# Kernel optimization log

Hardware: AMD Instinct MI355X
Metric: run time of the kernel (lower is better)

Reference implementation:

```python
import jax, jax.numpy as jnp
import numpy as np

B, L, S, D, H = 2, 384, 384, 512, 256
BASE_TEMP = 10.0
LN_EPS = 1e-5


def setup_inputs() -> dict:
    key = jax.random.key(0)
    ks = jax.random.split(key, 12)
    return {
        "q": jax.random.normal(ks[0], (B, L, D), jnp.float32),
        "k": jax.random.normal(ks[1], (B, S, D), jnp.float32),
        "q_global": jax.random.normal(ks[2], (B, D), jnp.float32),
        "k_global": jax.random.normal(ks[3], (B, D), jnp.float32),
        "W1": jax.random.normal(ks[4], (4 * D, H), jnp.float32) * (1.0 / np.sqrt(4 * D)),
        "b1": jnp.zeros((H,), jnp.float32),
        "gamma": jnp.ones((H,), jnp.float32),
        "beta": jnp.zeros((H,), jnp.float32),
        "W2": jax.random.normal(ks[5], (H, 1), jnp.float32) * (1.0 / np.sqrt(H)),
        "b2": jnp.zeros((1,), jnp.float32),
        "gumbel_u": jax.random.uniform(ks[6], (B, L, S, 2), jnp.float32),
    }


def reference(q, k, q_global, k_global, W1, b1, gamma, beta, W2, b2, gumbel_u):
    d = q.shape[-1]
    # Decompose Linear(4D,H) on the [q, k, q_global, k_global] concat into
    # four per-tensor projections; sum broadcasts to the pairwise grid.
    Wq, Wk, Wqg, Wkg = jnp.split(W1, 4, axis=0)  # each [D,H]
    hq = q @ Wq + (q_global @ Wqg)[:, None, :]   # [B,L,H]
    hk = k @ Wk + (k_global @ Wkg)[:, None, :]   # [B,S,H]
    h = hq[:, :, None, :] + hk[:, None, :, :] + b1  # [B,L,S,H]
    h = jax.nn.gelu(h, approximate=False)
    mu = jnp.mean(h, axis=-1, keepdims=True)
    var = jnp.mean(jnp.square(h - mu), axis=-1, keepdims=True)
    h = (h - mu) * jax.lax.rsqrt(var + LN_EPS) * gamma + beta
    thresholds = (h @ W2)[..., 0] + b2[0]  # [B,L,S]
    sim = jnp.einsum("bld,bsd->bls", q, k) / jnp.sqrt(jnp.float32(d))
    logits = (sim - thresholds) / BASE_TEMP
    binary_logits = jnp.stack([-logits, logits], axis=-1)  # [B,L,S,2]
    u = jnp.clip(gumbel_u, 1e-6, 1.0 - 1e-6)
    g = -jnp.log(-jnp.log(u))
    soft = jax.nn.softmax(binary_logits + g, axis=-1)  # tau=1.0
    hard = jax.nn.one_hot(jnp.argmax(soft, axis=-1), 2, dtype=soft.dtype)
    y = hard + soft - jax.lax.stop_gradient(soft)  # straight-through
    return y[..., 1][:, None, :, :]  # [B,1,L,S]
```

## Files before the change

kernel.cpp:

```cpp
#include <hip/hip_runtime.h>
#include <hip/hip_bf16.h>
#include <math.h>

#define Bb 2
#define Lq 384
#define Sk 384
#define Dd 512
#define Hh 256

#define PROJ_ROWS 2
#define LIST_CAP 65536

#define HQD_OFF  0
#define HKD_OFF  (HQD_OFF + Bb*Lq*Hh*8)
#define GQD_OFF  (HKD_OFF + Bb*Sk*Hh*8)
#define GKD_OFF  (GQD_OFF + Bb*Hh*8)
#define HQ_OFF   (GKD_OFF + Bb*Hh*8)
#define HK_OFF   (HQ_OFF + Bb*Lq*Hh*4)
#define SIM0_OFF (HK_OFF + Bb*Sk*Hh*4)
#define SIM1_OFF (SIM0_OFF + Bb*Lq*Sk*4)
#define CNT_OFF  (SIM1_OFF + Bb*Lq*Sk*4)
#define LIST_OFF (CNT_OFF + 16)

__global__ __launch_bounds__(256) void globald_kernel(
    const float* __restrict__ qg, const float* __restrict__ kg,
    const float* __restrict__ W1,
    double* __restrict__ gq_d, double* __restrict__ gk_d)
{
    __shared__ double red[64][5];
    int bx  = blockIdx.x;
    int isK = bx & 1;
    int b   = (bx >> 1) & 1;
    int hc  = bx >> 2;
    int tid = threadIdx.x;
    int hl  = tid >> 2;
    int dp  = tid & 3;
    int h   = hc * 64 + hl;
    const float* gv = (isK ? kg : qg) + b * Dd;
    const float* wp = W1 + (isK ? 3 : 2) * Dd * Hh + h;
    int d0 = dp * 128;
    double a0 = 0, a1 = 0, a2 = 0, a3 = 0;
    for (int i = 0; i < 128; i += 4) {
        int d = d0 + i;
        a0 = fma((double)gv[d + 0], (double)wp[(d + 0) * Hh], a0);
        a1 = fma((double)gv[d + 1], (double)wp[(d + 1) * Hh], a1);
        a2 = fma((double)gv[d + 2], (double)wp[(d + 2) * Hh], a2);
        a3 = fma((double)gv[d + 3], (double)wp[(d + 3) * Hh], a3);
    }
    red[hl][dp] = ((a0 + a1) + (a2 + a3));
    __syncthreads();
    if (dp == 0) {
        double s = (red[hl][0] + red[hl][1]) + (red[hl][2] + red[hl][3]);
        (isK ? gk_d : gq_d)[b * Hh + h] = s;
    }
}

__global__ __launch_bounds__(256) void projd_kernel(
    const float* __restrict__ q, const float* __restrict__ k,
    const float* __restrict__ W1, const float* __restrict__ b1,
    const double* __restrict__ gq_d, const double* __restrict__ gk_d,
    double* __restrict__ hq_d, double* __restrict__ hk_d,
    float* __restrict__ hq, float* __restrict__ hk)
{
    __shared__ __align__(16) float tile[PROJ_ROWS][Dd];
    int tid = threadIdx.x;
    const int tpb  = Lq / PROJ_ROWS;
    const int half = Bb * tpb;
    int bx = blockIdx.x;
    bool isQ = bx < half;
    int bb = isQ ? bx : bx - half;
    int b  = bb / tpb;
    int rt = bb % tpb;
    const float*  src = isQ ? q : k;
    const double* gl  = isQ ? gq_d : gk_d;
    int woff = isQ ? 0 : Dd * Hh;
    double* dstd = isQ ? hq_d : hk_d;
    float*  dstf = isQ ? hq : hk;

    int base = (b * Lq + rt * PROJ_ROWS) * Dd;
    *reinterpret_cast<float4*>(&tile[0][0] + tid * 4) =
        *reinterpret_cast<const float4*>(src + base + tid * 4);
    double gd = gl[b * Hh + tid];
    __syncthreads();

    const float* wp = W1 + woff + tid;
    double acc0 = 0.0, acc1 = 0.0;
    for (int d4 = 0; d4 < Dd; d4 += 4) {
        double w0 = (double)wp[(d4 + 0) * Hh];
        double w1 = (double)wp[(d4 + 1) * Hh];
        double w2 = (double)wp[(d4 + 2) * Hh];
        double w3 = (double)wp[(d4 + 3) * Hh];
        float4 t0 = *reinterpret_cast<const float4*>(&tile[0][d4]);
        float4 t1 = *reinterpret_cast<const float4*>(&tile[1][d4]);
        acc0 = fma((double)t0.x, w0, acc0);
        acc0 = fma((double)t0.y, w1, acc0);
        acc0 = fma((double)t0.z, w2, acc0);
        acc0 = fma((double)t0.w, w3, acc0);
        acc1 = fma((double)t1.x, w0, acc1);
        acc1 = fma((double)t1.y, w1, acc1);
        acc1 = fma((double)t1.z, w2, acc1);
        acc1 = fma((double)t1.w, w3, acc1);
    }
    double b1d = isQ ? (double)b1[tid] : 0.0;
    int ob = (b * Lq + rt * PROJ_ROWS) * Hh + tid;
    double tot0 = acc0 + gd, tot1 = acc1 + gd;
    dstd[ob]      = tot0;
    dstd[ob + Hh] = tot1;
    dstf[ob]      = (float)(tot0 + b1d);
    dstf[ob + Hh] = (float)(tot1 + b1d);
}

__global__ __launch_bounds__(256) void sim_kernel(
    const float* __restrict__ q, const float* __restrict__ k,
    float* __restrict__ sim01)
{
    __shared__ __align__(16) float qs[32][132];
    __shared__ __align__(16) float ks[32][132];
    int tid = threadIdx.x;
    int bx = blockIdx.x;
    int kc = (bx >= Bb * 144) ? 1 : 0;
    int r  = bx - kc * Bb * 144;
    int b  = r / 144;  r %= 144;
    int lt = r / 12, st = r % 12;
    int tl = tid >> 4, ts = tid & 15;
    const float* qb = q + (b * Lq + lt * 32) * Dd;
    const float* kb = k + (b * Sk + st * 32) * Dd;
    float a00 = 0.f, a01 = 0.f, a10 = 0.f, a11 = 0.f;
    for (int c = kc * 256; c < kc * 256 + 256; c += 128) {
        __syncthreads();
        for (int i = tid; i < 1024; i += 256) {
            int row = i >> 5;
            int c4  = (i & 31) << 2;
            *reinterpret_cast<float4*>(&qs[row][c4]) =
                *reinterpret_cast<const float4*>(qb + row * Dd + c + c4);
            *reinterpret_cast<float4*>(&ks[row][c4]) =
                *reinterpret_cast<const float4*>(kb + row * Dd + c + c4);
        }
        __syncthreads();
#pragma unroll 2
        for (int dd = 0; dd < 128; dd += 4) {
            float4 q0 = *reinterpret_cast<const float4*>(&qs[tl][dd]);
            float4 q1 = *reinterpret_cast<const float4*>(&qs[tl + 16][dd]);
            float4 k0 = *reinterpret_cast<const float4*>(&ks[ts][dd]);
            float4 k1 = *reinterpret_cast<const float4*>(&ks[ts + 16][dd]);
            a00 = fmaf(q0.x, k0.x, a00); a00 = fmaf(q0.y, k0.y, a00);
            a00 = fmaf(q0.z, k0.z, a00); a00 = fmaf(q0.w, k0.w, a00);
            a01 = fmaf(q0.x, k1.x, a01); a01 = fmaf(q0.y, k1.y, a01);
            a01 = fmaf(q0.z, k1.z, a01); a01 = fmaf(q0.w, k1.w, a01);
            a10 = fmaf(q1.x, k0.x, a10); a10 = fmaf(q1.y, k0.y, a10);
            a10 = fmaf(q1.z, k0.z, a10); a10 = fmaf(q1.w, k0.w, a10);
            a11 = fmaf(q1.x, k1.x, a11); a11 = fmaf(q1.y, k1.y, a11);
            a11 = fmaf(q1.z, k1.z, a11); a11 = fmaf(q1.w, k1.w, a11);
        }
    }
    const float sc = 0.04419417382415922f;
    float* dst = sim01 + kc * (Bb * Lq * Sk);
    int l0 = lt * 32 + tl, s0 = st * 32 + ts;
    dst[(b * Lq + l0)      * Sk + s0]      = a00 * sc;
    dst[(b * Lq + l0)      * Sk + s0 + 16] = a01 * sc;
    dst[(b * Lq + l0 + 16) * Sk + s0]      = a10 * sc;
    dst[(b * Lq + l0 + 16) * Sk + s0 + 16] = a11 * sc;
}

__global__ __launch_bounds__(256) void main_kernel(
    const float* __restrict__ hq, const float* __restrict__ hk,
    const float* __restrict__ sim0, const float* __restrict__ sim1,
    const float* __restrict__ gam, const float* __restrict__ bet,
    const float* __restrict__ W2, const float* __restrict__ b2,
    const float* __restrict__ gu, float* __restrict__ out,
    int* __restrict__ cnt, int* __restrict__ list)
{
    __shared__ __align__(16) float hq_t[16][258];
    __shared__ __align__(16) float hk_t[16][258];
    __shared__ __align__(16) float gw_s[256];
    __shared__ float2 red[256];
    int tid = threadIdx.x;
    int bx = blockIdx.x;
    int b  = bx / (24 * 24);
    int r  = bx % (24 * 24);
    int lt = r / 24, st = r % 24;

    const float* hqb = hq + (b * Lq + lt * 16) * Hh;
    const float* hkb = hk + (b * Sk + st * 16) * Hh;
#pragma unroll
    for (int kk = 0; kk < 16; ++kk) {
        hq_t[kk][tid] = hqb[kk * Hh + tid];
        hk_t[kk][tid] = hkb[kk * Hh + tid];
    }
    float w2v = W2[tid];
    float gwv = gam[tid] * w2v;
    gw_s[tid] = gwv;
    red[tid]  = make_float2(gwv, bet[tid] * w2v);
    __syncthreads();
    for (int o = 128; o > 0; o >>= 1) {
        if (tid < o) {
            red[tid].x += red[tid + o].x;
            red[tid].y += red[tid + o].y;
        }
        __syncthreads();
    }
    float gwsum  = red[0].x;
    float bconst = red[0].y + b2[0];

    const float C1  = 0.70710678118654752f;
    const float Pp  = 0.3275911f;
    const float A1f = 0.254829592f, A2f = -0.284496736f, A3f = 1.421413741f,
                A4f = -1.453152027f, A5f = 1.061405429f;
    const float NL2E = -1.442695040888963f;

    int tl = tid >> 4, ts = tid & 15;
    float s1 = 0.f, s2 = 0.f, sw = 0.f;
#pragma unroll 4
    for (int h2 = 0; h2 < 128; ++h2) {
        float2 hqv = *reinterpret_cast<const float2*>(&hq_t[tl][2 * h2]);
        float2 hkv = *reinterpret_cast<const float2*>(&hk_t[ts][2 * h2]);
        float2 gw2 = *reinterpret_cast<const float2*>(&gw_s[2 * h2]);
#pragma unroll
        for (int e = 0; e < 2; ++e) {
            float x  = (e == 0) ? (hqv.x + hkv.x) : (hqv.y + hkv.y);
            float gw = (e == 0) ? gw2.x : gw2.y;
            float ax = fabsf(x);
            float a  = C1 * ax;
            float dd = fmaf(Pp, a, 1.0f);
            float tt = __builtin_amdgcn_rcpf(dd);
            float ex = __builtin_amdgcn_exp2f(a * a * NL2E);
            float s  = fmaf(A5f, tt, A4f);
            s = fmaf(s, tt, A3f);
            s = fmaf(s, tt, A2f);
            s = fmaf(s, tt, A1f);
            s = s * tt;
            float E = fmaf(-s, ex, 1.0f);
            float y = fmaf(0.5f * ax, E, 0.5f * x);
            s1 += y;
            s2 = fmaf(y, y, s2);
            sw = fmaf(y, gw, sw);
        }
    }
    float mu   = s1 * (1.0f / 256.0f);
    float var  = s2 * (1.0f / 256.0f) - mu * mu;
    float rstd = rsqrtf(var + 1e-5f);
    float thr  = rstd * (sw - mu * gwsum) + bconst;

    int l = lt * 16 + tl, s = st * 16 + ts;
    int idx = (b * Lq + l) * Sk + s;
    float  sv = sim0[idx] + sim1[idx];
    float2 uv = reinterpret_cast<const float2*>(gu)[idx];
    float u0 = fminf(fmaxf(uv.x, 1e-6f), 1.0f - 1e-6f);
    float u1 = fminf(fmaxf(uv.y, 1e-6f), 1.0f - 1e-6f);
    float g0 = -logf(-logf(u0));
    float g1 = -logf(-logf(u1));
    float t  = 0.2f * (sv - thr) + (g1 - g0);
    out[idx] = t > 0.0f ? 1.0f : 0.0f;
    if (fabsf(t) < 1e-3f) {
        int p = atomicAdd(cnt, 1);
        if (p < LIST_CAP) list[p] = idx;
    }
}

__global__ __launch_bounds__(256) void cleanup_kernel(
    const float* __restrict__ q, const float* __restrict__ k,
    const double* __restrict__ hq_d, const double* __restrict__ hk_d,
    const float* __restrict__ b1,
    const float* __restrict__ gam, const float* __restrict__ bet,
    const float* __restrict__ W2, const float* __restrict__ b2,
    const float* __restrict__ gu, float* __restrict__ out,
    const int* __restrict__ cnt, const int* __restrict__ list)
{
    __shared__ double s0[256], s1[256], s2[256], s3[256];
    int tid = threadIdx.x;
    int n = *cnt;
    if (n > LIST_CAP) n = LIST_CAP;
    if (n == 0) return;

    double gw  = (double)gam[tid] * (double)W2[tid];
    double b1d = (double)b1[tid];
    s0[tid] = (double)bet[tid] * (double)W2[tid];
    s1[tid] = gw;
    __syncthreads();
    for (int o = 128; o > 0; o >>= 1) {
        if (tid < o) { s0[tid] += s0[tid + o]; s1[tid] += s1[tid + o]; }
        __syncthreads();
    }
    double bconst = s0[0] + (double)b2[0];
    double gwsum  = s1[0];
    __syncthreads();

    for (int it = blockIdx.x; it < n; it += gridDim.x) {
        int idx = list[it];
        int b   = idx / (Lq * Sk);
        int rem = idx % (Lq * Sk);
        int l = rem / Sk, s = rem % Sk;
        double x = (hq_d[(b * Lq + l) * Hh + tid]
                  + hk_d[(b * Sk + s) * Hh + tid]) + b1d;
        double y = 0.5 * x * (1.0 + erf(x * 0.70710678118654752440));
        const float* qrow = q + (b * Lq + l) * Dd;
        const float* krow = k + (b * Sk + s) * Dd;
        double sp = (double)qrow[tid] * (double)krow[tid]
                  + (double)qrow[tid + 256] * (double)krow[tid + 256];
        s0[tid] = y; s1[tid] = y * y; s2[tid] = y * gw; s3[tid] = sp;
        __syncthreads();
        for (int o = 128; o > 0; o >>= 1) {
            if (tid < o) {
                s0[tid] += s0[tid + o]; s1[tid] += s1[tid + o];
                s2[tid] += s2[tid + o]; s3[tid] += s3[tid + o];
            }
            __syncthreads();
        }
        if (tid == 0) {
            double mu   = s0[0] * (1.0 / 256.0);
            double var  = s1[0] * (1.0 / 256.0) - mu * mu;
            double rstd = 1.0 / sqrt(var + 1e-5);
            double thr  = rstd * (s2[0] - mu * gwsum) + bconst;
            double simv = s3[0] / 22.627416997969522;
            float2 uv = reinterpret_cast<const float2*>(gu)[idx];
            double u0 = fmin(fmax((double)uv.x, 1e-6), 1.0 - 1e-6);
            double u1 = fmin(fmax((double)uv.y, 1e-6), 1.0 - 1e-6);
            double g0 = -log(-log(u0));
            double g1 = -log(-log(u1));
            double t  = 0.2 * (simv - thr) + (g1 - g0);
            out[idx] = t > 0.0 ? 1.0f : 0.0f;
        }
        __syncthreads();
    }
}

extern "C" void kernel_launch(void* const* d_in, const int* in_sizes, int n_in,
                              void* d_out, int out_size, void* d_ws, size_t ws_size,
                              hipStream_t stream)
{
    const float* q   = (const float*)d_in[0];
    const float* k   = (const float*)d_in[1];
    const float* qg  = (const float*)d_in[2];
    const float* kg  = (const float*)d_in[3];
    const float* W1  = (const float*)d_in[4];
    const float* b1  = (const float*)d_in[5];
    const float* gam = (const float*)d_in[6];
    const float* bet = (const float*)d_in[7];
    const float* W2  = (const float*)d_in[8];
    const float* b2  = (const float*)d_in[9];
    const float* gu  = (const float*)d_in[10];
    float* out = (float*)d_out;

    char*   ws   = (char*)d_ws;
    double* hq_d = (double*)(ws + HQD_OFF);
    double* hk_d = (double*)(ws + HKD_OFF);
    double* gq_d = (double*)(ws + GQD_OFF);
    double* gk_d = (double*)(ws + GKD_OFF);
    float*  hq   = (float*)(ws + HQ_OFF);
    float*  hk   = (float*)(ws + HK_OFF);
    float*  sim0 = (float*)(ws + SIM0_OFF);
    float*  sim1 = (float*)(ws + SIM1_OFF);
    int*    cnt  = (int*)(ws + CNT_OFF);
    int*    list = (int*)(ws + LIST_OFF);

    hipMemsetAsync(cnt, 0, sizeof(int), stream);
    globald_kernel<<<16, 256, 0, stream>>>(qg, kg, W1, gq_d, gk_d);
    projd_kernel<<<2 * Bb * (Lq / PROJ_ROWS), 256, 0, stream>>>(
        q, k, W1, b1, gq_d, gk_d, hq_d, hk_d, hq, hk);
    sim_kernel<<<2 * Bb * 144, 256, 0, stream>>>(q, k, sim0);
    main_kernel<<<Bb * 24 * 24, 256, 0, stream>>>(
        hq, hk, sim0, sim1, gam, bet, W2, b2, gu, out, cnt, list);
    cleanup_kernel<<<768, 256, 0, stream>>>(
        q, k, hq_d, hk_d, b1, gam, bet, W2, b2, gu, out, cnt, list);
}
```

Measured before the change: 175.2 us.

## Reblock fp64 projection, hoist LN constants, and streamline GELU inner loop

The projection kernel now uses 512-thread blocks, each covering 8 rows with the D reduction split across two halves, so every W1 load is reused across more rows. The per-block gamma*W2 reduction moves out of main_kernel into a combined small kernel that writes the results to workspace. The GELU loop folds the 1/sqrt2 and 0.5 scalings into its constants, processes two lanes with independent accumulators and float4 shared loads, and pads rows to 260. The main risks are fewer projection blocks (192) lowering parallelism, and small floating-point changes near the decision threshold, which cleanup_kernel is meant to handle.

```diff
diff --git a/kernel.cpp b/kernel.cpp
--- a/kernel.cpp
+++ b/kernel.cpp
@@ -8,7 +8,6 @@
 #define Dd 512
 #define Hh 256
 
-#define PROJ_ROWS 2
 #define LIST_CAP 65536
 
 #define HQD_OFF  0
@@ -19,95 +18,134 @@
 #define HK_OFF   (HQ_OFF + Bb*Lq*Hh*4)
 #define SIM0_OFF (HK_OFF + Bb*Sk*Hh*4)
 #define SIM1_OFF (SIM0_OFF + Bb*Lq*Sk*4)
-#define CNT_OFF  (SIM1_OFF + Bb*Lq*Sk*4)
-#define LIST_OFF (CNT_OFF + 16)
-
-__global__ __launch_bounds__(256) void globald_kernel(
+#define SCAL_OFF (SIM1_OFF + Bb*Lq*Sk*4)
+#define GW_OFF   (SCAL_OFF + 64)
+#define CNT_OFF  (GW_OFF + 1024)
+#define LIST_OFF (CNT_OFF + 64)
+
+__global__ __launch_bounds__(256) void smalls_kernel(
     const float* __restrict__ qg, const float* __restrict__ kg,
     const float* __restrict__ W1,
-    double* __restrict__ gq_d, double* __restrict__ gk_d)
+    const float* __restrict__ gam, const float* __restrict__ bet,
+    const float* __restrict__ W2, const float* __restrict__ b2,
+    double* __restrict__ gq_d, double* __restrict__ gk_d,
+    float* __restrict__ gw_out, float* __restrict__ scal)
 {
     __shared__ double red[64][5];
+    __shared__ float2 red2[256];
     int bx  = blockIdx.x;
-    int isK = bx & 1;
-    int b   = (bx >> 1) & 1;
-    int hc  = bx >> 2;
     int tid = threadIdx.x;
-    int hl  = tid >> 2;
-    int dp  = tid & 3;
-    int h   = hc * 64 + hl;
-    const float* gv = (isK ? kg : qg) + b * Dd;
-    const float* wp = W1 + (isK ? 3 : 2) * Dd * Hh + h;
-    int d0 = dp * 128;
-    double a0 = 0, a1 = 0, a2 = 0, a3 = 0;
-    for (int i = 0; i < 128; i += 4) {
-        int d = d0 + i;
-        a0 = fma((double)gv[d + 0], (double)wp[(d + 0) * Hh], a0);
-        a1 = fma((double)gv[d + 1], (double)wp[(d + 1) * Hh], a1);
-        a2 = fma((double)gv[d + 2], (double)wp[(d + 2) * Hh], a2);
-        a3 = fma((double)gv[d + 3], (double)wp[(d + 3) * Hh], a3);
-    }
-    red[hl][dp] = ((a0 + a1) + (a2 + a3));
-    __syncthreads();
-    if (dp == 0) {
-        double s = (red[hl][0] + red[hl][1]) + (red[hl][2] + red[hl][3]);
-        (isK ? gk_d : gq_d)[b * Hh + h] = s;
-    }
-}
-
-__global__ __launch_bounds__(256) void projd_kernel(
+    if (bx < 16) {
+        int isK = bx & 1;
+        int b   = (bx >> 1) & 1;
+        int hc  = bx >> 2;
+        int hl  = tid >> 2;
+        int dp  = tid & 3;
+        int h   = hc * 64 + hl;
+        const float* gv = (isK ? kg : qg) + b * Dd;
+        const float* wp = W1 + (isK ? 3 : 2) * Dd * Hh + h;
+        int d0 = dp * 128;
+        double a0 = 0, a1 = 0, a2 = 0, a3 = 0;
+        for (int i = 0; i < 128; i += 4) {
+            int d = d0 + i;
+            a0 = fma((double)gv[d + 0], (double)wp[(d + 0) * Hh], a0);
+            a1 = fma((double)gv[d + 1], (double)wp[(d + 1) * Hh], a1);
+            a2 = fma((double)gv[d + 2], (double)wp[(d + 2) * Hh], a2);
+            a3 = fma((double)gv[d + 3], (double)wp[(d + 3) * Hh], a3);
+        }
+        red[hl][dp] = ((a0 + a1) + (a2 + a3));
+        __syncthreads();
+        if (dp == 0) {
+            double s = (red[hl][0] + red[hl][1]) + (red[hl][2] + red[hl][3]);
+            (isK ? gk_d : gq_d)[b * Hh + h] = s;
+        }
+    } else {
+        float w2v = W2[tid];
+        float gwv = gam[tid] * w2v;
+        gw_out[tid] = gwv;
+        red2[tid] = make_float2(gwv, bet[tid] * w2v);
+        __syncthreads();
+        for (int o = 128; o > 0; o >>= 1) {
+            if (tid < o) {
+                red2[tid].x += red2[tid + o].x;
+                red2[tid].y += red2[tid + o].y;
+            }
+            __syncthreads();
+        }
+        if (tid == 0) {
+            scal[0] = red2[0].x;
+            scal[1] = red2[0].y + b2[0];
+        }
+    }
+}
+
+__global__ __launch_bounds__(512) void projd_kernel(
     const float* __restrict__ q, const float* __restrict__ k,
     const float* __restrict__ W1, const float* __restrict__ b1,
     const double* __restrict__ gq_d, const double* __restrict__ gk_d,
     double* __restrict__ hq_d, double* __restrict__ hk_d,
     float* __restrict__ hq, float* __restrict__ hk)
 {
-    __shared__ __align__(16) float tile[PROJ_ROWS][Dd];
+    __shared__ __align__(16) float smem[8 * 512];
+    float  (*tile)[512] = (float (*)[512])smem;
+    double (*pbuf)[256] = (double (*)[256])smem;
     int tid = threadIdx.x;
-    const int tpb  = Lq / PROJ_ROWS;
-    const int half = Bb * tpb;
+    int h   = tid & 255;
+    int dh  = tid >> 8;
     int bx = blockIdx.x;
-    bool isQ = bx < half;
-    int bb = isQ ? bx : bx - half;
-    int b  = bb / tpb;
-    int rt = bb % tpb;
+    bool isQ = bx < 96;
+    int bb = isQ ? bx : bx - 96;
+    int b  = bb / 48;
+    int rg = bb % 48;
     const float*  src = isQ ? q : k;
     const double* gl  = isQ ? gq_d : gk_d;
     int woff = isQ ? 0 : Dd * Hh;
     double* dstd = isQ ? hq_d : hk_d;
     float*  dstf = isQ ? hq : hk;
 
-    int base = (b * Lq + rt * PROJ_ROWS) * Dd;
-    *reinterpret_cast<float4*>(&tile[0][0] + tid * 4) =
-        *reinterpret_cast<const float4*>(src + base + tid * 4);
-    double gd = gl[b * Hh + tid];
-    __syncthreads();
-
-    const float* wp = W1 + woff + tid;
-    double acc0 = 0.0, acc1 = 0.0;
-    for (int d4 = 0; d4 < Dd; d4 += 4) {
+    int base = (b * Lq + rg * 8) * Dd;
+    for (int i = tid; i < 1024; i += 512)
+        *reinterpret_cast<float4*>(&smem[i * 4]) =
+            *reinterpret_cast<const float4*>(src + base + i * 4);
+    __syncthreads();
+
+    const float* wp = W1 + woff + (dh * 256) * Hh + h;
+    int dbase = dh * 256;
+    double acc[8];
+#pragma unroll
+    for (int r = 0; r < 8; ++r) acc[r] = 0.0;
+#pragma unroll 2
+    for (int d4 = 0; d4 < 256; d4 += 4) {
         double w0 = (double)wp[(d4 + 0) * Hh];
         double w1 = (double)wp[(d4 + 1) * Hh];
         double w2 = (double)wp[(d4 + 2) * Hh];
         double w3 = (double)wp[(d4 + 3) * Hh];
-        float4 t0 = *reinterpret_cast<const float4*>(&tile[0][d4]);
-        float4 t1 = *reinterpret_cast<const float4*>(&tile[1][d4]);
-        acc0 = fma((double)t0.x, w0, acc0);
-        acc0 = fma((double)t0.y, w1, acc0);
-        acc0 = fma((double)t0.z, w2, acc0);
-        acc0 = fma((double)t0.w, w3, acc0);
-        acc1 = fma((double)t1.x, w0, acc1);
-        acc1 = fma((double)t1.y, w1, acc1);
-        acc1 = fma((double)t1.z, w2, acc1);
-        acc1 = fma((double)t1.w, w3, acc1);
-    }
-    double b1d = isQ ? (double)b1[tid] : 0.0;
-    int ob = (b * Lq + rt * PROJ_ROWS) * Hh + tid;
-    double tot0 = acc0 + gd, tot1 = acc1 + gd;
-    dstd[ob]      = tot0;
-    dstd[ob + Hh] = tot1;
-    dstf[ob]      = (float)(tot0 + b1d);
-    dstf[ob + Hh] = (float)(tot1 + b1d);
+#pragma unroll
+        for (int r = 0; r < 8; ++r) {
+            float4 tv = *reinterpret_cast<const float4*>(&tile[r][dbase + d4]);
+            acc[r] = fma((double)tv.x, w0, acc[r]);
+            acc[r] = fma((double)tv.y, w1, acc[r]);
+            acc[r] = fma((double)tv.z, w2, acc[r]);
+            acc[r] = fma((double)tv.w, w3, acc[r]);
+        }
+    }
+    __syncthreads();
+    if (dh == 1) {
+#pragma unroll
+        for (int r = 0; r < 8; ++r) pbuf[r][h] = acc[r];
+    }
+    __syncthreads();
+    if (dh == 0) {
+        double gd  = gl[b * Hh + h];
+        double b1d = isQ ? (double)b1[h] : 0.0;
+        int ob = (b * Lq + rg * 8) * Hh + h;
+#pragma unroll
+        for (int r = 0; r < 8; ++r) {
+            double tot = (acc[r] + pbuf[r][h]) + gd;
+            dstd[ob + r * Hh] = tot;
+            dstf[ob + r * Hh] = (float)(tot + b1d);
+        }
+    }
 }
 
 __global__ __launch_bounds__(256) void sim_kernel(
@@ -162,18 +200,43 @@
     dst[(b * Lq + l0 + 16) * Sk + s0 + 16] = a11 * sc;
 }
 
+__device__ __forceinline__ void gelu2(float2 hqv, float2 hkv, float2 gwv,
+                                      float2& s1, float2& s2, float2& sw)
+{
+    const float P2   = 0.23164189f;
+    const float A1f = 0.254829592f, A2f = -0.284496736f, A3f = 1.421413741f,
+                A4f = -1.453152027f, A5f = 1.061405429f;
+    const float NL2EH = -0.72134752044448170f;
+
+    float xa = hqv.x + hkv.x,        xb = hqv.y + hkv.y;
+    float axa = fabsf(xa),           axb = fabsf(xb);
+    float dda = fmaf(P2, axa, 1.0f), ddb = fmaf(P2, axb, 1.0f);
+    float ta = __builtin_amdgcn_rcpf(dda), tb = __builtin_amdgcn_rcpf(ddb);
+    float x2a = xa * xa,             x2b = xb * xb;
+    float exa = __builtin_amdgcn_exp2f(x2a * NL2EH);
+    float exb = __builtin_amdgcn_exp2f(x2b * NL2EH);
+    float sa = fmaf(A5f, ta, A4f),   sb = fmaf(A5f, tb, A4f);
+    sa = fmaf(sa, ta, A3f);          sb = fmaf(sb, tb, A3f);
+    sa = fmaf(sa, ta, A2f);          sb = fmaf(sb, tb, A2f);
+    sa = fmaf(sa, ta, A1f);          sb = fmaf(sb, tb, A1f);
+    sa = sa * ta;                    sb = sb * tb;
+    float Ea = fmaf(-sa, exa, 1.0f), Eb = fmaf(-sb, exb, 1.0f);
+    float ya = fmaf(axa, Ea, xa),    yb = fmaf(axb, Eb, xb);
+    s1.x += ya;                      s1.y += yb;
+    s2.x = fmaf(ya, ya, s2.x);       s2.y = fmaf(yb, yb, s2.y);
+    sw.x = fmaf(ya, gwv.x, sw.x);    sw.y = fmaf(yb, gwv.y, sw.y);
+}
+
 __global__ __launch_bounds__(256) void main_kernel(
     const float* __restrict__ hq, const float* __restrict__ hk,
     const float* __restrict__ sim0, const float* __restrict__ sim1,
-    const float* __restrict__ gam, const float* __restrict__ bet,
-    const float* __restrict__ W2, const float* __restrict__ b2,
+    const float* __restrict__ gw_in, const float* __restrict__ scal,
     const float* __restrict__ gu, float* __restrict__ out,
     int* __restrict__ cnt, int* __restrict__ list)
 {
-    __shared__ __align__(16) float hq_t[16][258];
-    __shared__ __align__(16) float hk_t[16][258];
+    __shared__ __align__(16) float hq_t[16][260];
+    __shared__ __align__(16) float hk_t[16][260];
     __shared__ __align__(16) float gw_s[256];
-    __shared__ float2 red[256];
     int tid = threadIdx.x;
     int bx = blockIdx.x;
     int b  = bx / (24 * 24);
@@ -183,63 +246,41 @@
     const float* hqb = hq + (b * Lq + lt * 16) * Hh;
     const float* hkb = hk + (b * Sk + st * 16) * Hh;
 #pragma unroll
-    for (int kk = 0; kk < 16; ++kk) {
-        hq_t[kk][tid] = hqb[kk * Hh + tid];
-        hk_t[kk][tid] = hkb[kk * Hh + tid];
-    }
-    float w2v = W2[tid];
-    float gwv = gam[tid] * w2v;
-    gw_s[tid] = gwv;
-    red[tid]  = make_float2(gwv, bet[tid] * w2v);
-    __syncthreads();
-    for (int o = 128; o > 0; o >>= 1) {
-        if (tid < o) {
-            red[tid].x += red[tid + o].x;
-            red[tid].y += red[tid + o].y;
-        }
-        __syncthreads();
-    }
-    float gwsum  = red[0].x;
-    float bconst = red[0].y + b2[0];
-
-    const float C1  = 0.70710678118654752f;
-    const float Pp  = 0.3275911f;
-    const float A1f = 0.254829592f, A2f = -0.284496736f, A3f = 1.421413741f,
-                A4f = -1.453152027f, A5f = 1.061405429f;
-    const float NL2E = -1.442695040888963f;
+    for (int i = 0; i < 4; ++i) {
+        int idx4 = i * 256 + tid;
+        int row  = idx4 >> 6;
+        int col4 = (idx4 & 63) << 2;
+        *reinterpret_cast<float4*>(&hq_t[row][col4]) =
+            *reinterpret_cast<const float4*>(hqb + row * Hh + col4);
+        *reinterpret_cast<float4*>(&hk_t[row][col4]) =
+            *reinterpret_cast<const float4*>(hkb + row * Hh + col4);
+    }
+    gw_s[tid] = gw_in[tid];
+    __syncthreads();
+    float gwsum  = scal[0];
+    float bconst = scal[1];
 
     int tl = tid >> 4, ts = tid & 15;
-    float s1 = 0.f, s2 = 0.f, sw = 0.f;
-#pragma unroll 4
-    for (int h2 = 0; h2 < 128; ++h2) {
-        float2 hqv = *reinterpret_cast<const float2*>(&hq_t[tl][2 * h2]);
-        float2 hkv = *reinterpret_cast<const float2*>(&hk_t[ts][2 * h2]);
-        float2 gw2 = *reinterpret_cast<const float2*>(&gw_s[2 * h2]);
-#pragma unroll
-        for (int e = 0; e < 2; ++e) {
-            float x  = (e == 0) ? (hqv.x + hkv.x) : (hqv.y + hkv.y);
-            float gw = (e == 0) ? gw2.x : gw2.y;
-            float ax = fabsf(x);
-            float a  = C1 * ax;
-            float dd = fmaf(Pp, a, 1.0f);
-            float tt = __builtin_amdgcn_rcpf(dd);
-            float ex = __builtin_amdgcn_exp2f(a * a * NL2E);
-            float s  = fmaf(A5f, tt, A4f);
-            s = fmaf(s, tt, A3f);
-            s = fmaf(s, tt, A2f);
-            s = fmaf(s, tt, A1f);
-            s = s * tt;
-            float E = fmaf(-s, ex, 1.0f);
-            float y = fmaf(0.5f * ax, E, 0.5f * x);
-            s1 += y;
-            s2 = fmaf(y, y, s2);
-            sw = fmaf(y, gw, sw);
-        }
-    }
-    float mu   = s1 * (1.0f / 256.0f);
-    float var  = s2 * (1.0f / 256.0f) - mu * mu;
+    float2 s1 = make_float2(0.f, 0.f);
+    float2 s2 = make_float2(0.f, 0.f);
+    float2 sw = make_float2(0.f, 0.f);
+#pragma unroll 2
+    for (int h4 = 0; h4 < Hh; h4 += 4) {
+        float4 hq4 = *reinterpret_cast<const float4*>(&hq_t[tl][h4]);
+        float4 hk4 = *reinterpret_cast<const float4*>(&hk_t[ts][h4]);
+        float4 gw4 = *reinterpret_cast<const float4*>(&gw_s[h4]);
+        gelu2(make_float2(hq4.x, hq4.y), make_float2(hk4.x, hk4.y),
+              make_float2(gw4.x, gw4.y), s1, s2, sw);
+        gelu2(make_float2(hq4.z, hq4.w), make_float2(hk4.z, hk4.w),
+              make_float2(gw4.z, gw4.w), s1, s2, sw);
+    }
+    float S1 = s1.x + s1.y;
+    float S2 = s2.x + s2.y;
+    float SW = 0.5f * (sw.x + sw.y);
+    float mu   = S1 * (1.0f / 512.0f);
+    float var  = S2 * (1.0f / 1024.0f) - mu * mu;
     float rstd = rsqrtf(var + 1e-5f);
-    float thr  = rstd * (sw - mu * gwsum) + bconst;
+    float thr  = rstd * (SW - mu * gwsum) + bconst;
 
     int l = lt * 16 + tl, s = st * 16 + ts;
     int idx = (b * Lq + l) * Sk + s;
@@ -350,16 +391,19 @@
     float*  hk   = (float*)(ws + HK_OFF);
     float*  sim0 = (float*)(ws + SIM0_OFF);
     float*  sim1 = (float*)(ws + SIM1_OFF);
+    float*  scal = (float*)(ws + SCAL_OFF);
+    float*  gw   = (float*)(ws + GW_OFF);
     int*    cnt  = (int*)(ws + CNT_OFF);
     int*    list = (int*)(ws + LIST_OFF);
 
     hipMemsetAsync(cnt, 0, sizeof(int), stream);
-    globald_kernel<<<16, 256, 0, stream>>>(qg, kg, W1, gq_d, gk_d);
-    projd_kernel<<<2 * Bb * (Lq / PROJ_ROWS), 256, 0, stream>>>(
+    smalls_kernel<<<17, 256, 0, stream>>>(
+        qg, kg, W1, gam, bet, W2, b2, gq_d, gk_d, gw, scal);
+    projd_kernel<<<192, 512, 0, stream>>>(
         q, k, W1, b1, gq_d, gk_d, hq_d, hk_d, hq, hk);
     sim_kernel<<<2 * Bb * 144, 256, 0, stream>>>(q, k, sim0);
     main_kernel<<<Bb * 24 * 24, 256, 0, stream>>>(
-        hq, hk, sim0, sim1, gam, bet, W2, b2, gu, out, cnt, list);
+        hq, hk, sim0, sim1, gw, scal, gu, out, cnt, list);
     cleanup_kernel<<<768, 256, 0, stream>>>(
         q, k, hq_d, hk_d, b1, gam, bet, W2, b2, gu, out, cnt, list);
 }
```

Result: faster. 167.6 us (-4.4%).
